# Performance work log

Measured on AMD Instinct MI355X. Metric: run time of the kernel, lower is better.

Reference implementation:

```python
import jax, jax.numpy as jnp
import numpy as np

N, E, G = 50000, 600000, 512
F_IN, H, OUT = 128, 128, 256


def setup_inputs() -> dict:
    key = jax.random.key(0)
    ks = jax.random.split(key, 16)
    x = jax.random.normal(ks[0], (N, F_IN), dtype=jnp.float32)
    edge_index = jax.random.randint(ks[1], (2, E), 0, N, dtype=jnp.int64)
    batch = jnp.sort(jax.random.randint(ks[2], (N,), 0, G, dtype=jnp.int64))
    def lin(k, out_d, in_d):
        s = 1.0 / np.sqrt(in_d)
        return jax.random.uniform(k, (out_d, in_d), jnp.float32, -s, s)
    W1l, W1r = lin(ks[3], H, F_IN), lin(ks[4], H, F_IN)
    b1 = jnp.zeros((H,), jnp.float32)
    W2l, W2r = lin(ks[5], H, H), lin(ks[6], H, H)
    b2 = jnp.zeros((H,), jnp.float32)
    W3l, W3r = lin(ks[7], H, H), lin(ks[8], H, H)
    b3 = jnp.zeros((H,), jnp.float32)
    Wlin = lin(ks[9], OUT, 2 * H)
    blin = jnp.zeros((OUT,), jnp.float32)
    return dict(x=x, edge_index=edge_index, batch=batch,
                W1l=W1l, b1=b1, W1r=W1r, W2l=W2l, b2=b2, W2r=W2r,
                W3l=W3l, b3=b3, W3r=W3r, Wlin=Wlin, blin=blin)


def reference(x, edge_index, batch, W1l, b1, W1r, W2l, b2, W2r, W3l, b3, W3r, Wlin, blin):
    src, dst = edge_index[0], edge_index[1]
    # in-degree of each target node (mean aggregation denominator)
    deg = jax.ops.segment_sum(jnp.ones((E,), x.dtype), dst, num_segments=N)
    deg = jnp.maximum(deg, 1.0)[:, None]

    def sage(h, Wl, bl, Wr):
        # mean-aggregate neighbor features then linear; plus root transform
        agg = jax.ops.segment_sum(h[src], dst, num_segments=N) / deg
        return agg @ Wl.T + bl + h @ Wr.T

    h = jax.nn.relu(sage(x, W1l, b1, W1r))
    h = jax.nn.relu(sage(h, W2l, b2, W2r))
    h = sage(h, W3l, b3, W3r)

    # global max / mean pool per graph
    x_max = jax.ops.segment_max(h, batch, num_segments=G)
    x_max = jnp.where(jnp.isfinite(x_max), x_max, 0.0)
    cnt = jnp.maximum(jax.ops.segment_sum(jnp.ones((N,), h.dtype), batch, num_segments=G), 1.0)
    x_mean = jax.ops.segment_sum(h, batch, num_segments=G) / cnt[:, None]

    pooled = jnp.concatenate([x_max, x_mean], axis=1)  # [G, 2H]
    # dropout is identity in eval mode
    return pooled @ Wlin.T + blin
```

## Files before the change

### kernel.cpp

```cpp
#include <hip/hip_runtime.h>
#include <hip/hip_bf16.h>
#include <hip/hip_fp16.h>


#define FH 128
#define OUTD 256
#define SCHUNK 2048

typedef unsigned int u32;
typedef unsigned short u16;
typedef __attribute__((ext_vector_type(8))) _Float16 f16frag;
typedef __attribute__((ext_vector_type(4))) float f4frag;

typedef __attribute__((address_space(3))) u32 lds_u32;
typedef __attribute__((address_space(1))) const u32 glb_u32;

__device__ inline void async_copy16(const void* g, void* l) {
    __builtin_amdgcn_global_load_lds((glb_u32*)g, (lds_u32*)l, 16, 0, 0);
}

__global__ void prep_all(const float* __restrict__ x, u16* __restrict__ x16, int n4, int PX,
                         const float* __restrict__ W0, const float* __restrict__ W1,
                         const float* __restrict__ W2, const float* __restrict__ W3,
                         const float* __restrict__ W4, const float* __restrict__ W5,
                         uint4* __restrict__ Bf, int PW,
                         const int* __restrict__ dst, int* __restrict__ cnt, int E) {
    int blk = blockIdx.x;
    if (blk < PX) {
        int id = blk * 256 + threadIdx.x;
        if (id >= n4) return;
        float4 v = *(const float4*)(x + (size_t)id * 4);
        __half h0 = __float2half(v.x), h1 = __float2half(v.y);
        __half h2 = __float2half(v.z), h3 = __float2half(v.w);
        ushort4 s;
        s.x = *(u16*)&h0; s.y = *(u16*)&h1; s.z = *(u16*)&h2; s.w = *(u16*)&h3;
        *(ushort4*)(x16 + (size_t)id * 4) = s;
    } else if (blk < PX + PW) {
        int pair = (blk - PX) * 4 + (threadIdx.x >> 6);
        if (pair >= 48) return;
        int ks = pair & 7;
        int arr = pair >> 3;
        int l = threadIdx.x & 63;
        const float* Ws[6] = {W0, W1, W2, W3, W4, W5};
        const float* W = Ws[arr];
        bool use_lo = (ks >= 4);
        int kb = (ks & 3) * 32 + (l >> 4) * 8;
        uint4* out = Bf + (size_t)arr * 4096;
        #pragma unroll
        for (int ot = 0; ot < 8; ++ot) {
            int o = ot * 16 + (l & 15);
            u32 h[8];
            #pragma unroll
            for (int i = 0; i < 8; ++i) {
                float v = W[o * 128 + kb + i];
                __half hi = __float2half(v);
                if (use_lo) {
                    float rem = v - __half2float(hi);
                    __half lo = __float2half(rem);
                    h[i] = *(u16*)&lo;
                } else {
                    h[i] = *(u16*)&hi;
                }
            }
            uint4 u;
            u.x = h[0] | (h[1] << 16);
            u.y = h[2] | (h[3] << 16);
            u.z = h[4] | (h[5] << 16);
            u.w = h[6] | (h[7] << 16);
            out[(ks * 8 + ot) * 64 + l] = u;
        }
    } else {
        int e = (blk - PX - PW) * 256 + threadIdx.x;
        if (e < E) atomicAdd(&cnt[dst[e]], 1);
    }
}

__global__ void scanA_kernel(const int* __restrict__ cnt, int* __restrict__ bsum, int n) {
    __shared__ int ws[4];
    int b = blockIdx.x, t = threadIdx.x;
    int base = b * SCHUNK + t * 8;
    int s = 0;
    #pragma unroll
    for (int k = 0; k < 8; ++k) {
        int i = base + k;
        s += (i < n) ? cnt[i] : 0;
    }
    #pragma unroll
    for (int off = 32; off >= 1; off >>= 1) s += __shfl_xor(s, off, 64);
    int w = t >> 6, lane = t & 63;
    if (lane == 0) ws[w] = s;
    __syncthreads();
    if (t == 0) bsum[b] = ws[0] + ws[1] + ws[2] + ws[3];
}

__global__ void scanC_kernel(const int* __restrict__ cnt, const int* __restrict__ bsum,
                             int NB, int* __restrict__ rp, float* __restrict__ dinv, int n) {
    __shared__ int ws[4];
    __shared__ int base_s;
    int b = blockIdx.x, t = threadIdx.x;
    if (t < 64) {
        int v = (t < NB) ? bsum[t] : 0;
        int pre = (t < b) ? v : 0;
        #pragma unroll
        for (int off = 32; off >= 1; off >>= 1) pre += __shfl_xor(pre, off, 64);
        if (t == 0) base_s = pre;
        if (b == 0) {
            int tot = v;
            #pragma unroll
            for (int off = 32; off >= 1; off >>= 1) tot += __shfl_xor(tot, off, 64);
            if (t == 0) rp[n] = tot;
        }
    }
    __syncthreads();
    int boff = base_s;
    int base = b * SCHUNK + t * 8;
    int v[8];
    int ts = 0;
    #pragma unroll
    for (int k = 0; k < 8; ++k) {
        int i = base + k;
        v[k] = (i < n) ? cnt[i] : 0;
        ts += v[k];
    }
    int w = t >> 6, lane = t & 63;
    int x = ts;
    #pragma unroll
    for (int off = 1; off < 64; off <<= 1) {
        int y = __shfl_up(x, off, 64);
        if (lane >= off) x += y;
    }
    if (lane == 63) ws[w] = x;
    __syncthreads();
    int woff = 0;
    #pragma unroll
    for (int q = 0; q < 4; ++q) woff += (q < w) ? ws[q] : 0;
    int run = boff + woff + (x - ts);
    #pragma unroll
    for (int k = 0; k < 8; ++k) {
        int i = base + k;
        if (i < n) {
            rp[i] = run;
            dinv[i] = 1.0f / (float)max(v[k], 1);
        }
        run += v[k];
    }
}

__global__ void scatter_bounds(const int* __restrict__ src, const int* __restrict__ dst,
                               const int* __restrict__ rp, int* __restrict__ cursor,
                               int* __restrict__ esrc, int E, int SC,
                               const int* __restrict__ batch, int* __restrict__ gstart,
                               int n, int g) {
    int blk = blockIdx.x;
    if (blk < SC) {
        int e = blk * 256 + threadIdx.x;
        if (e < E) {
            int d = dst[e];
            int pos = rp[d] + atomicAdd(&cursor[d], 1);
            esrc[pos] = src[e];
        }
    } else {
        int i = (blk - SC) * 256 + threadIdx.x;
        if (i >= n) return;
        int b = batch[i];
        int pb = (i == 0) ? -1 : batch[i - 1];
        for (int q = pb + 1; q <= b; ++q) gstart[q] = i;
        if (i == n - 1) {
            for (int q = b + 1; q <= g; ++q) gstart[q] = n;
        }
    }
}

__device__ inline void add8(float* a, uint4 u) {
    float2 f0 = __half22float2(*(__half2*)&u.x);
    float2 f1 = __half22float2(*(__half2*)&u.y);
    float2 f2 = __half22float2(*(__half2*)&u.z);
    float2 f3 = __half22float2(*(__half2*)&u.w);
    a[0] += f0.x; a[1] += f0.y; a[2] += f1.x; a[3] += f1.y;
    a[4] += f2.x; a[5] += f2.y; a[6] += f3.x; a[7] += f3.y;
}

__global__ void agg_kernel(const u16* __restrict__ h16,
                           const int* __restrict__ rp, const int* __restrict__ esrc,
                           const float* __restrict__ dinv,
                           u16* __restrict__ agg16, int n_nodes) {
    int node = blockIdx.x * 16 + (threadIdx.x >> 4);
    if (node >= n_nodes) return;
    int lane = threadIdx.x & 15;
    int f = lane * 8;
    int s0 = rp[node], s1 = rp[node + 1];
    float a0[8] = {0, 0, 0, 0, 0, 0, 0, 0};
    float a1[8] = {0, 0, 0, 0, 0, 0, 0, 0};
    float a2[8] = {0, 0, 0, 0, 0, 0, 0, 0};
    float a3[8] = {0, 0, 0, 0, 0, 0, 0, 0};
    int j = s0;
    for (; j + 8 <= s1; j += 8) {
        int i0 = esrc[j],     i1 = esrc[j + 1], i2 = esrc[j + 2], i3 = esrc[j + 3];
        int i4 = esrc[j + 4], i5 = esrc[j + 5], i6 = esrc[j + 6], i7 = esrc[j + 7];
        uint4 u0 = *(const uint4*)(h16 + (size_t)i0 * FH + f);
        uint4 u1 = *(const uint4*)(h16 + (size_t)i1 * FH + f);
        uint4 u2 = *(const uint4*)(h16 + (size_t)i2 * FH + f);
        uint4 u3 = *(const uint4*)(h16 + (size_t)i3 * FH + f);
        uint4 u4 = *(const uint4*)(h16 + (size_t)i4 * FH + f);
        uint4 u5 = *(const uint4*)(h16 + (size_t)i5 * FH + f);
        uint4 u6 = *(const uint4*)(h16 + (size_t)i6 * FH + f);
        uint4 u7 = *(const uint4*)(h16 + (size_t)i7 * FH + f);
        add8(a0, u0); add8(a1, u1); add8(a2, u2); add8(a3, u3);
        add8(a0, u4); add8(a1, u5); add8(a2, u6); add8(a3, u7);
    }
    if (j + 4 <= s1) {
        int i0 = esrc[j], i1 = esrc[j + 1], i2 = esrc[j + 2], i3 = esrc[j + 3];
        uint4 u0 = *(const uint4*)(h16 + (size_t)i0 * FH + f);
        uint4 u1 = *(const uint4*)(h16 + (size_t)i1 * FH + f);
        uint4 u2 = *(const uint4*)(h16 + (size_t)i2 * FH + f);
        uint4 u3 = *(const uint4*)(h16 + (size_t)i3 * FH + f);
        add8(a0, u0); add8(a1, u1); add8(a2, u2); add8(a3, u3);
        j += 4;
    }
    for (; j < s1; ++j) {
        uint4 u0 = *(const uint4*)(h16 + (size_t)esrc[j] * FH + f);
        add8(a0, u0);
    }
    float di = dinv[node];
    u32 oh[8];
    #pragma unroll
    for (int i = 0; i < 8; ++i) {
        __half hv = __float2half((a0[i] + a1[i] + a2[i] + a3[i]) * di);
        oh[i] = *(u16*)&hv;
    }
    uint4 w;
    w.x = oh[0] | (oh[1] << 16);
    w.y = oh[2] | (oh[3] << 16);
    w.z = oh[4] | (oh[5] << 16);
    w.w = oh[6] | (oh[7] << 16);
    *(uint4*)(agg16 + (size_t)node * FH + f) = w;
}

__global__ __launch_bounds__(256, 2)
void mfma_gemm(const u16* __restrict__ A1, const u16* __restrict__ A2,
               const uint4* __restrict__ Bf1, const uint4* __restrict__ Bf2,
               const float* __restrict__ bias, u16* __restrict__ out16,
               int do_relu) {
    __shared__ uint4 Bl[4096];
    int tid = threadIdx.x;
    int l = tid & 63;
    int wv = tid >> 6;
    int bn0 = blockIdx.x * 192 + wv * 48;
    int m = l & 15, q = l >> 4;

    f4frag acc[3][8];
    #pragma unroll
    for (int i = 0; i < 3; ++i)
        #pragma unroll
        for (int o = 0; o < 8; ++o)
            acc[i][o] = (f4frag){0.f, 0.f, 0.f, 0.f};

    #pragma unroll
    for (int p = 0; p < 2; ++p) {
        const u16* P = p ? A2 : A1;
        const uint4* Bf = p ? Bf2 : Bf1;

        f16frag Af[3][4];
        #pragma unroll
        for (int nt = 0; nt < 3; ++nt)
            #pragma unroll
            for (int s = 0; s < 4; ++s)
                Af[nt][s] = *(const f16frag*)(P + (size_t)(bn0 + nt * 16 + m) * FH + s * 32 + q * 8);

        __syncthreads();

        #pragma unroll
        for (int u = 0; u < 16; ++u)
            async_copy16(Bf + (size_t)u * 256 + wv * 64 + l,
                         &Bl[u * 256 + wv * 64]);
        __syncthreads();

        #pragma unroll
        for (int s = 0; s < 4; ++s) {
            {
                f16frag B[8];
                #pragma unroll
                for (int ot = 0; ot < 8; ++ot)
                    B[ot] = *(const f16frag*)&Bl[(size_t)(s * 8 + ot) * 64 + l];
                #pragma unroll
                for (int ot = 0; ot < 8; ++ot)
                    #pragma unroll
                    for (int nt = 0; nt < 3; ++nt)
                        acc[nt][ot] = __builtin_amdgcn_mfma_f32_16x16x32_f16(Af[nt][s], B[ot], acc[nt][ot], 0, 0, 0);
            }
            {
                f16frag B[8];
                #pragma unroll
                for (int ot = 0; ot < 8; ++ot)
                    B[ot] = *(const f16frag*)&Bl[(size_t)((s + 4) * 8 + ot) * 64 + l];
                #pragma unroll
                for (int ot = 0; ot < 8; ++ot)
                    #pragma unroll
                    for (int nt = 0; nt < 3; ++nt)
                        acc[nt][ot] = __builtin_amdgcn_mfma_f32_16x16x32_f16(Af[nt][s], B[ot], acc[nt][ot], 0, 0, 0);
            }
        }
    }

    #pragma unroll
    for (int nt = 0; nt < 3; ++nt)
        #pragma unroll
        for (int r = 0; r < 4; ++r) {
            int node = bn0 + nt * 16 + q * 4 + r;
            #pragma unroll
            for (int ot = 0; ot < 8; ++ot) {
                float v = acc[nt][ot][r] + bias[ot * 16 + m];
                if (do_relu) v = fmaxf(v, 0.f);
                __half hv = __float2half(v);
                out16[(size_t)node * FH + ot * 16 + m] = *(u16*)&hv;
            }
        }
}

__global__ __launch_bounds__(256, 2)
void pool_final(const u16* __restrict__ h16, const int* __restrict__ gstart,
                const float* __restrict__ Wlin, const float* __restrict__ blin,
                float* __restrict__ out) {
    __shared__ float smax[16][FH];
    __shared__ float ssum[16][FH];
    __shared__ float pr[2 * FH];
    int g = blockIdx.x;
    int tid = threadIdx.x;
    int way = tid >> 4;
    int lane = tid & 15;
    int f = lane * 8;
    int s = gstart[g], e = gstart[g + 1];

    float mx[8], sm[8];
    #pragma unroll
    for (int i = 0; i < 8; ++i) { mx[i] = -INFINITY; sm[i] = 0.f; }
    for (int n = s + way; n < e; n += 16) {
        uint4 u = *(const uint4*)(h16 + (size_t)n * FH + f);
        float2 f0 = __half22float2(*(__half2*)&u.x);
        float2 f1 = __half22float2(*(__half2*)&u.y);
        float2 f2 = __half22float2(*(__half2*)&u.z);
        float2 f3 = __half22float2(*(__half2*)&u.w);
        float v[8] = {f0.x, f0.y, f1.x, f1.y, f2.x, f2.y, f3.x, f3.y};
        #pragma unroll
        for (int i = 0; i < 8; ++i) {
            mx[i] = fmaxf(mx[i], v[i]);
            sm[i] += v[i];
        }
    }
    #pragma unroll
    for (int i = 0; i < 8; ++i) {
        smax[way][f + i] = mx[i];
        ssum[way][f + i] = sm[i];
    }
    __syncthreads();
    int c = e - s;
    if (tid < FH) {
        float m2 = -INFINITY, s2 = 0.f;
        #pragma unroll
        for (int w2 = 0; w2 < 16; ++w2) {
            m2 = fmaxf(m2, smax[w2][tid]);
            s2 += ssum[w2][tid];
        }
        pr[tid] = (c > 0) ? m2 : 0.f;
        pr[FH + tid] = s2 / (float)max(c, 1);
    }
    __syncthreads();
    int o = tid;
    const float4* wr = (const float4*)(Wlin + (size_t)o * (2 * FH));
    float acc = 0.f;
    #pragma unroll
    for (int j = 0; j < (2 * FH) / 4; ++j) {
        float4 wv = wr[j];
        acc += wv.x * pr[j * 4 + 0] + wv.y * pr[j * 4 + 1] +
               wv.z * pr[j * 4 + 2] + wv.w * pr[j * 4 + 3];
    }
    out[(size_t)g * OUTD + o] = acc + blin[o];
}

extern "C" void kernel_launch(void* const* d_in, const int* in_sizes, int n_in,
                              void* d_out, int out_size, void* d_ws, size_t ws_size,
                              hipStream_t stream) {
    const float* x     = (const float*)d_in[0];
    const int*   ei    = (const int*)d_in[1];
    const int*   batch = (const int*)d_in[2];
    const float* W1l = (const float*)d_in[3];
    const float* b1  = (const float*)d_in[4];
    const float* W1r = (const float*)d_in[5];
    const float* W2l = (const float*)d_in[6];
    const float* b2  = (const float*)d_in[7];
    const float* W2r = (const float*)d_in[8];
    const float* W3l = (const float*)d_in[9];
    const float* b3  = (const float*)d_in[10];
    const float* W3r = (const float*)d_in[11];
    const float* Wlin = (const float*)d_in[12];
    const float* blin = (const float*)d_in[13];
    float* out = (float*)d_out;

    const int E = in_sizes[1] / 2;
    const int N = in_sizes[2];
    const int G = out_size / OUTD;
    const int* src = ei;
    const int* dst = ei + E;
    const int NB = (N + SCHUNK - 1) / SCHUNK;
    const int GB = (N + 191) / 192;
    const int NP = GB * 192;

    char* w = (char*)d_ws;
    auto alloc = [&](size_t bytes) {
        void* p = (void*)w;
        w += (bytes + 255) & ~(size_t)255;
        return p;
    };
    int*   cnt    = (int*)alloc((size_t)2 * N * sizeof(int));
    int*   cursor = cnt + N;
    int*   rp     = (int*)alloc((size_t)(N + 1) * sizeof(int));
    int*   esrc   = (int*)alloc((size_t)E * sizeof(int));
    int*   gstart = (int*)alloc((size_t)(G + 1) * sizeof(int));
    float* dinv   = (float*)alloc((size_t)N * sizeof(float));
    int*   bsum   = (int*)alloc(64 * sizeof(int));
    u16*   x16    = (u16*)alloc((size_t)NP * FH * sizeof(u16));
    u16*   agg16  = (u16*)alloc((size_t)NP * FH * sizeof(u16));
    u16*   hA16   = (u16*)alloc((size_t)NP * FH * sizeof(u16));
    u16*   hB16   = (u16*)alloc((size_t)NP * FH * sizeof(u16));
    uint4* BF     = (uint4*)alloc((size_t)6 * 4096 * sizeof(uint4));
    (void)ws_size;

    hipMemsetAsync(cnt, 0, (size_t)2 * N * sizeof(int), stream);
    const int n4 = N * 32;
    const int PX = (n4 + 255) / 256;
    const int PW = 12;
    const int PH = (E + 255) / 256;
    prep_all<<<PX + PW + PH, 256, 0, stream>>>(x, x16, n4, PX,
                                               W1l, W1r, W2l, W2r, W3l, W3r, BF, PW,
                                               dst, cnt, E);

    scanA_kernel<<<NB, 256, 0, stream>>>(cnt, bsum, N);
    scanC_kernel<<<NB, 256, 0, stream>>>(cnt, bsum, NB, rp, dinv, N);
    const int SC = (E + 255) / 256;
    const int GBND = (N + 255) / 256;
    scatter_bounds<<<SC + GBND, 256, 0, stream>>>(src, dst, rp, cursor, esrc, E, SC,
                                                  batch, gstart, N, G);

    const int agg_grid = (N + 15) / 16;

    agg_kernel<<<agg_grid, 256, 0, stream>>>(x16, rp, esrc, dinv, agg16, N);
    mfma_gemm<<<GB, 256, 0, stream>>>(agg16, x16, BF + 0 * 4096, BF + 1 * 4096, b1, hA16, 1);
    agg_kernel<<<agg_grid, 256, 0, stream>>>(hA16, rp, esrc, dinv, agg16, N);
    mfma_gemm<<<GB, 256, 0, stream>>>(agg16, hA16, BF + 2 * 4096, BF + 3 * 4096, b2, hB16, 1);
    agg_kernel<<<agg_grid, 256, 0, stream>>>(hB16, rp, esrc, dinv, agg16, N);
    mfma_gemm<<<GB, 256, 0, stream>>>(agg16, hB16, BF + 4 * 4096, BF + 5 * 4096, b3, hA16, 0);

    pool_final<<<G, 256, 0, stream>>>(hA16, gstart, Wlin, blin, out);
}
```

Before: 324.2 us.

## Fuse neighbor aggregation into GEMM kernel via LDS and merge scan kernels

The separate agg_kernel and mfma_gemm launches are merged into one agg_gemm kernel. Each block gathers and mean-aggregates its 192 nodes' neighbor features into swizzled LDS, then runs the MFMA GEMM on that tile. This removes the agg16 global write and read round trip and three launches. The two-pass scan is also collapsed into one kernel, where each block redundantly sums its whole prefix. In exchange, the gather phase now runs at GEMM-sized occupancy with only 261 blocks and 12 serial node passes per wave group, which may hide gather latency less well.

```diff
diff --git a/kernel.cpp b/kernel.cpp
--- a/kernel.cpp
+++ b/kernel.cpp
@@ -75,44 +75,26 @@
     }
 }
 
-__global__ void scanA_kernel(const int* __restrict__ cnt, int* __restrict__ bsum, int n) {
+__global__ void scan_kernel(const int* __restrict__ cnt, int* __restrict__ rp,
+                            float* __restrict__ dinv, int n) {
     __shared__ int ws[4];
     int b = blockIdx.x, t = threadIdx.x;
-    int base = b * SCHUNK + t * 8;
-    int s = 0;
-    #pragma unroll
-    for (int k = 0; k < 8; ++k) {
-        int i = base + k;
-        s += (i < n) ? cnt[i] : 0;
-    }
-    #pragma unroll
-    for (int off = 32; off >= 1; off >>= 1) s += __shfl_xor(s, off, 64);
     int w = t >> 6, lane = t & 63;
-    if (lane == 0) ws[w] = s;
-    __syncthreads();
-    if (t == 0) bsum[b] = ws[0] + ws[1] + ws[2] + ws[3];
-}
-
-__global__ void scanC_kernel(const int* __restrict__ cnt, const int* __restrict__ bsum,
-                             int NB, int* __restrict__ rp, float* __restrict__ dinv, int n) {
-    __shared__ int ws[4];
-    __shared__ int base_s;
-    int b = blockIdx.x, t = threadIdx.x;
-    if (t < 64) {
-        int v = (t < NB) ? bsum[t] : 0;
-        int pre = (t < b) ? v : 0;
-        #pragma unroll
-        for (int off = 32; off >= 1; off >>= 1) pre += __shfl_xor(pre, off, 64);
-        if (t == 0) base_s = pre;
-        if (b == 0) {
-            int tot = v;
-            #pragma unroll
-            for (int off = 32; off >= 1; off >>= 1) tot += __shfl_xor(tot, off, 64);
-            if (t == 0) rp[n] = tot;
-        }
-    }
-    __syncthreads();
-    int boff = base_s;
+
+    int pre = 0;
+    const int4* c4 = (const int4*)cnt;
+    int npre4 = (b * SCHUNK) >> 2;
+    for (int i = t; i < npre4; i += 256) {
+        int4 v = c4[i];
+        pre += v.x + v.y + v.z + v.w;
+    }
+    #pragma unroll
+    for (int off = 32; off >= 1; off >>= 1) pre += __shfl_xor(pre, off, 64);
+    if (lane == 0) ws[w] = pre;
+    __syncthreads();
+    int boff = ws[0] + ws[1] + ws[2] + ws[3];
+    __syncthreads();
+
     int base = b * SCHUNK + t * 8;
     int v[8];
     int ts = 0;
@@ -122,7 +104,6 @@
         v[k] = (i < n) ? cnt[i] : 0;
         ts += v[k];
     }
-    int w = t >> 6, lane = t & 63;
     int x = ts;
     #pragma unroll
     for (int off = 1; off < 64; off <<= 1) {
@@ -144,6 +125,7 @@
         }
         run += v[k];
     }
+    if (b == (int)gridDim.x - 1 && t == 255) rp[n] = run;
 }
 
 __global__ void scatter_bounds(const int* __restrict__ src, const int* __restrict__ dst,
@@ -180,73 +162,91 @@
     a[4] += f2.x; a[5] += f2.y; a[6] += f3.x; a[7] += f3.y;
 }
 
-__global__ void agg_kernel(const u16* __restrict__ h16,
-                           const int* __restrict__ rp, const int* __restrict__ esrc,
-                           const float* __restrict__ dinv,
-                           u16* __restrict__ agg16, int n_nodes) {
-    int node = blockIdx.x * 16 + (threadIdx.x >> 4);
-    if (node >= n_nodes) return;
-    int lane = threadIdx.x & 15;
-    int f = lane * 8;
-    int s0 = rp[node], s1 = rp[node + 1];
-    float a0[8] = {0, 0, 0, 0, 0, 0, 0, 0};
-    float a1[8] = {0, 0, 0, 0, 0, 0, 0, 0};
-    float a2[8] = {0, 0, 0, 0, 0, 0, 0, 0};
-    float a3[8] = {0, 0, 0, 0, 0, 0, 0, 0};
-    int j = s0;
-    for (; j + 8 <= s1; j += 8) {
-        int i0 = esrc[j],     i1 = esrc[j + 1], i2 = esrc[j + 2], i3 = esrc[j + 3];
-        int i4 = esrc[j + 4], i5 = esrc[j + 5], i6 = esrc[j + 6], i7 = esrc[j + 7];
-        uint4 u0 = *(const uint4*)(h16 + (size_t)i0 * FH + f);
-        uint4 u1 = *(const uint4*)(h16 + (size_t)i1 * FH + f);
-        uint4 u2 = *(const uint4*)(h16 + (size_t)i2 * FH + f);
-        uint4 u3 = *(const uint4*)(h16 + (size_t)i3 * FH + f);
-        uint4 u4 = *(const uint4*)(h16 + (size_t)i4 * FH + f);
-        uint4 u5 = *(const uint4*)(h16 + (size_t)i5 * FH + f);
-        uint4 u6 = *(const uint4*)(h16 + (size_t)i6 * FH + f);
-        uint4 u7 = *(const uint4*)(h16 + (size_t)i7 * FH + f);
-        add8(a0, u0); add8(a1, u1); add8(a2, u2); add8(a3, u3);
-        add8(a0, u4); add8(a1, u5); add8(a2, u6); add8(a3, u7);
-    }
-    if (j + 4 <= s1) {
-        int i0 = esrc[j], i1 = esrc[j + 1], i2 = esrc[j + 2], i3 = esrc[j + 3];
-        uint4 u0 = *(const uint4*)(h16 + (size_t)i0 * FH + f);
-        uint4 u1 = *(const uint4*)(h16 + (size_t)i1 * FH + f);
-        uint4 u2 = *(const uint4*)(h16 + (size_t)i2 * FH + f);
-        uint4 u3 = *(const uint4*)(h16 + (size_t)i3 * FH + f);
-        add8(a0, u0); add8(a1, u1); add8(a2, u2); add8(a3, u3);
-        j += 4;
-    }
-    for (; j < s1; ++j) {
-        uint4 u0 = *(const uint4*)(h16 + (size_t)esrc[j] * FH + f);
-        add8(a0, u0);
-    }
-    float di = dinv[node];
-    u32 oh[8];
-    #pragma unroll
-    for (int i = 0; i < 8; ++i) {
-        __half hv = __float2half((a0[i] + a1[i] + a2[i] + a3[i]) * di);
-        oh[i] = *(u16*)&hv;
-    }
-    uint4 w;
-    w.x = oh[0] | (oh[1] << 16);
-    w.y = oh[2] | (oh[3] << 16);
-    w.z = oh[4] | (oh[5] << 16);
-    w.w = oh[6] | (oh[7] << 16);
-    *(uint4*)(agg16 + (size_t)node * FH + f) = w;
-}
-
 __global__ __launch_bounds__(256, 2)
-void mfma_gemm(const u16* __restrict__ A1, const u16* __restrict__ A2,
-               const uint4* __restrict__ Bf1, const uint4* __restrict__ Bf2,
-               const float* __restrict__ bias, u16* __restrict__ out16,
-               int do_relu) {
+void agg_gemm(const u16* __restrict__ H,
+              const int* __restrict__ rp, const int* __restrict__ esrc,
+              const float* __restrict__ dinv,
+              const uint4* __restrict__ Bf1, const uint4* __restrict__ Bf2,
+              const float* __restrict__ bias, u16* __restrict__ out16,
+              int do_relu, int n_nodes) {
     __shared__ uint4 Bl[4096];
+    u16* Al = (u16*)Bl;
     int tid = threadIdx.x;
+    int nbase = blockIdx.x * 192;
+
+    {
+        int way = tid >> 4;
+        int lane16 = tid & 15;
+        int f = lane16 * 8;
+        for (int p = 0; p < 12; ++p) {
+            int nl = p * 16 + way;
+            int node = nbase + nl;
+            int s0 = 0, s1 = 0;
+            float di = 0.f;
+            if (node < n_nodes) { s0 = rp[node]; s1 = rp[node + 1]; di = dinv[node]; }
+            float a0[8] = {0, 0, 0, 0, 0, 0, 0, 0};
+            float a1[8] = {0, 0, 0, 0, 0, 0, 0, 0};
+            float a2[8] = {0, 0, 0, 0, 0, 0, 0, 0};
+            float a3[8] = {0, 0, 0, 0, 0, 0, 0, 0};
+            int j = s0;
+            for (; j + 8 <= s1; j += 8) {
+                int i0 = esrc[j],     i1 = esrc[j + 1], i2 = esrc[j + 2], i3 = esrc[j + 3];
+                int i4 = esrc[j + 4], i5 = esrc[j + 5], i6 = esrc[j + 6], i7 = esrc[j + 7];
+                uint4 u0 = *(const uint4*)(H + (size_t)i0 * FH + f);
+                uint4 u1 = *(const uint4*)(H + (size_t)i1 * FH + f);
+                uint4 u2 = *(const uint4*)(H + (size_t)i2 * FH + f);
+                uint4 u3 = *(const uint4*)(H + (size_t)i3 * FH + f);
+                uint4 u4 = *(const uint4*)(H + (size_t)i4 * FH + f);
+                uint4 u5 = *(const uint4*)(H + (size_t)i5 * FH + f);
+                uint4 u6 = *(const uint4*)(H + (size_t)i6 * FH + f);
+                uint4 u7 = *(const uint4*)(H + (size_t)i7 * FH + f);
+                add8(a0, u0); add8(a1, u1); add8(a2, u2); add8(a3, u3);
+                add8(a0, u4); add8(a1, u5); add8(a2, u6); add8(a3, u7);
+            }
+            if (j + 4 <= s1) {
+                int i0 = esrc[j], i1 = esrc[j + 1], i2 = esrc[j + 2], i3 = esrc[j + 3];
+                uint4 u0 = *(const uint4*)(H + (size_t)i0 * FH + f);
+                uint4 u1 = *(const uint4*)(H + (size_t)i1 * FH + f);
+                uint4 u2 = *(const uint4*)(H + (size_t)i2 * FH + f);
+                uint4 u3 = *(const uint4*)(H + (size_t)i3 * FH + f);
+                add8(a0, u0); add8(a1, u1); add8(a2, u2); add8(a3, u3);
+                j += 4;
+            }
+            for (; j < s1; ++j) {
+                uint4 u0 = *(const uint4*)(H + (size_t)esrc[j] * FH + f);
+                add8(a0, u0);
+            }
+            u32 oh[8];
+            #pragma unroll
+            for (int i = 0; i < 8; ++i) {
+                __half hv = __float2half((a0[i] + a1[i] + a2[i] + a3[i]) * di);
+                oh[i] = *(u16*)&hv;
+            }
+            uint4 wv4;
+            wv4.x = oh[0] | (oh[1] << 16);
+            wv4.y = oh[2] | (oh[3] << 16);
+            wv4.z = oh[4] | (oh[5] << 16);
+            wv4.w = oh[6] | (oh[7] << 16);
+            int byte = (nl * 256 + lane16 * 16) ^ ((nl & 7) << 4);
+            *(uint4*)((char*)Al + byte) = wv4;
+        }
+    }
+    __syncthreads();
+
     int l = tid & 63;
     int wv = tid >> 6;
-    int bn0 = blockIdx.x * 192 + wv * 48;
+    int bn0 = nbase + wv * 48;
     int m = l & 15, q = l >> 4;
+
+    f16frag Af[3][4];
+    #pragma unroll
+    for (int nt = 0; nt < 3; ++nt)
+        #pragma unroll
+        for (int s = 0; s < 4; ++s) {
+            int nl = wv * 48 + nt * 16 + m;
+            int byte = (nl * 256 + s * 64 + q * 16) ^ ((nl & 7) << 4);
+            Af[nt][s] = *(const f16frag*)((const char*)Al + byte);
+        }
 
     f4frag acc[3][8];
     #pragma unroll
@@ -255,50 +255,78 @@
         for (int o = 0; o < 8; ++o)
             acc[i][o] = (f4frag){0.f, 0.f, 0.f, 0.f};
 
-    #pragma unroll
-    for (int p = 0; p < 2; ++p) {
-        const u16* P = p ? A2 : A1;
-        const uint4* Bf = p ? Bf2 : Bf1;
-
-        f16frag Af[3][4];
-        #pragma unroll
-        for (int nt = 0; nt < 3; ++nt)
-            #pragma unroll
-            for (int s = 0; s < 4; ++s)
-                Af[nt][s] = *(const f16frag*)(P + (size_t)(bn0 + nt * 16 + m) * FH + s * 32 + q * 8);
-
-        __syncthreads();
-
-        #pragma unroll
-        for (int u = 0; u < 16; ++u)
-            async_copy16(Bf + (size_t)u * 256 + wv * 64 + l,
-                         &Bl[u * 256 + wv * 64]);
-        __syncthreads();
-
-        #pragma unroll
-        for (int s = 0; s < 4; ++s) {
-            {
-                f16frag B[8];
+    __syncthreads();
+
+    #pragma unroll
+    for (int u = 0; u < 16; ++u)
+        async_copy16(Bf1 + (size_t)u * 256 + wv * 64 + l,
+                     &Bl[u * 256 + wv * 64]);
+    __syncthreads();
+
+    #pragma unroll
+    for (int s = 0; s < 4; ++s) {
+        {
+            f16frag B[8];
+            #pragma unroll
+            for (int ot = 0; ot < 8; ++ot)
+                B[ot] = *(const f16frag*)&Bl[(size_t)(s * 8 + ot) * 64 + l];
+            #pragma unroll
+            for (int ot = 0; ot < 8; ++ot)
                 #pragma unroll
-                for (int ot = 0; ot < 8; ++ot)
-                    B[ot] = *(const f16frag*)&Bl[(size_t)(s * 8 + ot) * 64 + l];
+                for (int nt = 0; nt < 3; ++nt)
+                    acc[nt][ot] = __builtin_amdgcn_mfma_f32_16x16x32_f16(Af[nt][s], B[ot], acc[nt][ot], 0, 0, 0);
+        }
+        {
+            f16frag B[8];
+            #pragma unroll
+            for (int ot = 0; ot < 8; ++ot)
+                B[ot] = *(const f16frag*)&Bl[(size_t)((s + 4) * 8 + ot) * 64 + l];
+            #pragma unroll
+            for (int ot = 0; ot < 8; ++ot)
                 #pragma unroll
-                for (int ot = 0; ot < 8; ++ot)
-                    #pragma unroll
-                    for (int nt = 0; nt < 3; ++nt)
-                        acc[nt][ot] = __builtin_amdgcn_mfma_f32_16x16x32_f16(Af[nt][s], B[ot], acc[nt][ot], 0, 0, 0);
-            }
-            {
-                f16frag B[8];
+                for (int nt = 0; nt < 3; ++nt)
+                    acc[nt][ot] = __builtin_amdgcn_mfma_f32_16x16x32_f16(Af[nt][s], B[ot], acc[nt][ot], 0, 0, 0);
+        }
+    }
+
+    f16frag Ag[3][4];
+    #pragma unroll
+    for (int nt = 0; nt < 3; ++nt)
+        #pragma unroll
+        for (int s = 0; s < 4; ++s)
+            Ag[nt][s] = *(const f16frag*)(H + (size_t)(bn0 + nt * 16 + m) * FH + s * 32 + q * 8);
+
+    __syncthreads();
+
+    #pragma unroll
+    for (int u = 0; u < 16; ++u)
+        async_copy16(Bf2 + (size_t)u * 256 + wv * 64 + l,
+                     &Bl[u * 256 + wv * 64]);
+    __syncthreads();
+
+    #pragma unroll
+    for (int s = 0; s < 4; ++s) {
+        {
+            f16frag B[8];
+            #pragma unroll
+            for (int ot = 0; ot < 8; ++ot)
+                B[ot] = *(const f16frag*)&Bl[(size_t)(s * 8 + ot) * 64 + l];
+            #pragma unroll
+            for (int ot = 0; ot < 8; ++ot)
                 #pragma unroll
-                for (int ot = 0; ot < 8; ++ot)
-                    B[ot] = *(const f16frag*)&Bl[(size_t)((s + 4) * 8 + ot) * 64 + l];
+                for (int nt = 0; nt < 3; ++nt)
+                    acc[nt][ot] = __builtin_amdgcn_mfma_f32_16x16x32_f16(Ag[nt][s], B[ot], acc[nt][ot], 0, 0, 0);
+        }
+        {
+            f16frag B[8];
+            #pragma unroll
+            for (int ot = 0; ot < 8; ++ot)
+                B[ot] = *(const f16frag*)&Bl[(size_t)((s + 4) * 8 + ot) * 64 + l];
+            #pragma unroll
+            for (int ot = 0; ot < 8; ++ot)
                 #pragma unroll
-                for (int ot = 0; ot < 8; ++ot)
-                    #pragma unroll
-                    for (int nt = 0; nt < 3; ++nt)
-                        acc[nt][ot] = __builtin_amdgcn_mfma_f32_16x16x32_f16(Af[nt][s], B[ot], acc[nt][ot], 0, 0, 0);
-            }
+                for (int nt = 0; nt < 3; ++nt)
+                    acc[nt][ot] = __builtin_amdgcn_mfma_f32_16x16x32_f16(Ag[nt][s], B[ot], acc[nt][ot], 0, 0, 0);
         }
     }
 
@@ -417,9 +445,7 @@
     int*   esrc   = (int*)alloc((size_t)E * sizeof(int));
     int*   gstart = (int*)alloc((size_t)(G + 1) * sizeof(int));
     float* dinv   = (float*)alloc((size_t)N * sizeof(float));
-    int*   bsum   = (int*)alloc(64 * sizeof(int));
     u16*   x16    = (u16*)alloc((size_t)NP * FH * sizeof(u16));
-    u16*   agg16  = (u16*)alloc((size_t)NP * FH * sizeof(u16));
     u16*   hA16   = (u16*)alloc((size_t)NP * FH * sizeof(u16));
     u16*   hB16   = (u16*)alloc((size_t)NP * FH * sizeof(u16));
     uint4* BF     = (uint4*)alloc((size_t)6 * 4096 * sizeof(uint4));
@@ -434,21 +460,15 @@
                                                W1l, W1r, W2l, W2r, W3l, W3r, BF, PW,
                                                dst, cnt, E);
 
-    scanA_kernel<<<NB, 256, 0, stream>>>(cnt, bsum, N);
-    scanC_kernel<<<NB, 256, 0, stream>>>(cnt, bsum, NB, rp, dinv, N);
+    scan_kernel<<<NB, 256, 0, stream>>>(cnt, rp, dinv, N);
     const int SC = (E + 255) / 256;
     const int GBND = (N + 255) / 256;
     scatter_bounds<<<SC + GBND, 256, 0, stream>>>(src, dst, rp, cursor, esrc, E, SC,
                                                   batch, gstart, N, G);
 
-    const int agg_grid = (N + 15) / 16;
-
-    agg_kernel<<<agg_grid, 256, 0, stream>>>(x16, rp, esrc, dinv, agg16, N);
-    mfma_gemm<<<GB, 256, 0, stream>>>(agg16, x16, BF + 0 * 4096, BF + 1 * 4096, b1, hA16, 1);
-    agg_kernel<<<agg_grid, 256, 0, stream>>>(hA16, rp, esrc, dinv, agg16, N);
-    mfma_gemm<<<GB, 256, 0, stream>>>(agg16, hA16, BF + 2 * 4096, BF + 3 * 4096, b2, hB16, 1);
-    agg_kernel<<<agg_grid, 256, 0, stream>>>(hB16, rp, esrc, dinv, agg16, N);
-    mfma_gemm<<<GB, 256, 0, stream>>>(agg16, hB16, BF + 4 * 4096, BF + 5 * 4096, b3, hA16, 0);
+    agg_gemm<<<GB, 256, 0, stream>>>(x16,  rp, esrc, dinv, BF + 0 * 4096, BF + 1 * 4096, b1, hA16, 1, N);
+    agg_gemm<<<GB, 256, 0, stream>>>(hA16, rp, esrc, dinv, BF + 2 * 4096, BF + 3 * 4096, b2, hB16, 1, N);
+    agg_gemm<<<GB, 256, 0, stream>>>(hB16, rp, esrc, dinv, BF + 4 * 4096, BF + 5 * 4096, b3, hA16, 0, N);
 
     pool_final<<<G, 256, 0, stream>>>(hA16, gstart, Wlin, blin, out);
 }
```

Measured after the change: 395.0 us. +21.8%, slower.

## Merge two-pass scan into one kernel and read GEMM weights from global directly

Applied to the files above, without the earlier changes.

The two scan kernels become one: each block sums all preceding counts itself (redundant prefix reads over at most ~50K ints) instead of going through a separate block-sum pass, which saves one launch. The GEMM drops the LDS staging of the weight fragments, so the async copy and both barriers are gone, and B fragments are loaded straight from global memory, relying on L1/L2 since every block reads the same 64KB of weights. The risk is higher global load latency inside the MFMA loop, set against lower LDS use and possibly higher occupancy.

```diff
diff --git a/kernel.cpp b/kernel.cpp
--- a/kernel.cpp
+++ b/kernel.cpp
@@ -11,13 +11,6 @@
 typedef unsigned short u16;
 typedef __attribute__((ext_vector_type(8))) _Float16 f16frag;
 typedef __attribute__((ext_vector_type(4))) float f4frag;
-
-typedef __attribute__((address_space(3))) u32 lds_u32;
-typedef __attribute__((address_space(1))) const u32 glb_u32;
-
-__device__ inline void async_copy16(const void* g, void* l) {
-    __builtin_amdgcn_global_load_lds((glb_u32*)g, (lds_u32*)l, 16, 0, 0);
-}
 
 __global__ void prep_all(const float* __restrict__ x, u16* __restrict__ x16, int n4, int PX,
                          const float* __restrict__ W0, const float* __restrict__ W1,
@@ -75,44 +68,26 @@
     }
 }
 
-__global__ void scanA_kernel(const int* __restrict__ cnt, int* __restrict__ bsum, int n) {
+__global__ void scan_kernel(const int* __restrict__ cnt, int* __restrict__ rp,
+                            float* __restrict__ dinv, int n) {
     __shared__ int ws[4];
     int b = blockIdx.x, t = threadIdx.x;
-    int base = b * SCHUNK + t * 8;
-    int s = 0;
-    #pragma unroll
-    for (int k = 0; k < 8; ++k) {
-        int i = base + k;
-        s += (i < n) ? cnt[i] : 0;
-    }
-    #pragma unroll
-    for (int off = 32; off >= 1; off >>= 1) s += __shfl_xor(s, off, 64);
     int w = t >> 6, lane = t & 63;
-    if (lane == 0) ws[w] = s;
+
+    int pre = 0;
+    const int4* c4 = (const int4*)cnt;
+    int npre4 = (b * SCHUNK) >> 2;
+    for (int i = t; i < npre4; i += 256) {
+        int4 v = c4[i];
+        pre += v.x + v.y + v.z + v.w;
+    }
+    #pragma unroll
+    for (int off = 32; off >= 1; off >>= 1) pre += __shfl_xor(pre, off, 64);
+    if (lane == 0) ws[w] = pre;
     __syncthreads();
-    if (t == 0) bsum[b] = ws[0] + ws[1] + ws[2] + ws[3];
-}
-
-__global__ void scanC_kernel(const int* __restrict__ cnt, const int* __restrict__ bsum,
-                             int NB, int* __restrict__ rp, float* __restrict__ dinv, int n) {
-    __shared__ int ws[4];
-    __shared__ int base_s;
-    int b = blockIdx.x, t = threadIdx.x;
-    if (t < 64) {
-        int v = (t < NB) ? bsum[t] : 0;
-        int pre = (t < b) ? v : 0;
-        #pragma unroll
-        for (int off = 32; off >= 1; off >>= 1) pre += __shfl_xor(pre, off, 64);
-        if (t == 0) base_s = pre;
-        if (b == 0) {
-            int tot = v;
-            #pragma unroll
-            for (int off = 32; off >= 1; off >>= 1) tot += __shfl_xor(tot, off, 64);
-            if (t == 0) rp[n] = tot;
-        }
-    }
+    int boff = ws[0] + ws[1] + ws[2] + ws[3];
     __syncthreads();
-    int boff = base_s;
+
     int base = b * SCHUNK + t * 8;
     int v[8];
     int ts = 0;
@@ -122,7 +97,6 @@
         v[k] = (i < n) ? cnt[i] : 0;
         ts += v[k];
     }
-    int w = t >> 6, lane = t & 63;
     int x = ts;
     #pragma unroll
     for (int off = 1; off < 64; off <<= 1) {
@@ -144,6 +118,7 @@
         }
         run += v[k];
     }
+    if (b == (int)gridDim.x - 1 && t == 255) rp[n] = run;
 }
 
 __global__ void scatter_bounds(const int* __restrict__ src, const int* __restrict__ dst,
@@ -241,7 +216,6 @@
                const uint4* __restrict__ Bf1, const uint4* __restrict__ Bf2,
                const float* __restrict__ bias, u16* __restrict__ out16,
                int do_relu) {
-    __shared__ uint4 Bl[4096];
     int tid = threadIdx.x;
     int l = tid & 63;
     int wv = tid >> 6;
@@ -267,32 +241,14 @@
             for (int s = 0; s < 4; ++s)
                 Af[nt][s] = *(const f16frag*)(P + (size_t)(bn0 + nt * 16 + m) * FH + s * 32 + q * 8);
 
-        __syncthreads();
-
-        #pragma unroll
-        for (int u = 0; u < 16; ++u)
-            async_copy16(Bf + (size_t)u * 256 + wv * 64 + l,
-                         &Bl[u * 256 + wv * 64]);
-        __syncthreads();
-
         #pragma unroll
         for (int s = 0; s < 4; ++s) {
-            {
+            #pragma unroll
+            for (int ph = 0; ph < 2; ++ph) {
                 f16frag B[8];
                 #pragma unroll
                 for (int ot = 0; ot < 8; ++ot)
-                    B[ot] = *(const f16frag*)&Bl[(size_t)(s * 8 + ot) * 64 + l];
-                #pragma unroll
-                for (int ot = 0; ot < 8; ++ot)
-                    #pragma unroll
-                    for (int nt = 0; nt < 3; ++nt)
-                        acc[nt][ot] = __builtin_amdgcn_mfma_f32_16x16x32_f16(Af[nt][s], B[ot], acc[nt][ot], 0, 0, 0);
-            }
-            {
-                f16frag B[8];
-                #pragma unroll
-                for (int ot = 0; ot < 8; ++ot)
-                    B[ot] = *(const f16frag*)&Bl[(size_t)((s + 4) * 8 + ot) * 64 + l];
+                    B[ot] = *(const f16frag*)&Bf[(size_t)((s + ph * 4) * 8 + ot) * 64 + l];
                 #pragma unroll
                 for (int ot = 0; ot < 8; ++ot)
                     #pragma unroll
@@ -417,7 +373,6 @@
     int*   esrc   = (int*)alloc((size_t)E * sizeof(int));
     int*   gstart = (int*)alloc((size_t)(G + 1) * sizeof(int));
     float* dinv   = (float*)alloc((size_t)N * sizeof(float));
-    int*   bsum   = (int*)alloc(64 * sizeof(int));
     u16*   x16    = (u16*)alloc((size_t)NP * FH * sizeof(u16));
     u16*   agg16  = (u16*)alloc((size_t)NP * FH * sizeof(u16));
     u16*   hA16   = (u16*)alloc((size_t)NP * FH * sizeof(u16));
@@ -434,8 +389,7 @@
                                                W1l, W1r, W2l, W2r, W3l, W3r, BF, PW,
                                                dst, cnt, E);
 
-    scanA_kernel<<<NB, 256, 0, stream>>>(cnt, bsum, N);
-    scanC_kernel<<<NB, 256, 0, stream>>>(cnt, bsum, NB, rp, dinv, N);
+    scan_kernel<<<NB, 256, 0, stream>>>(cnt, rp, dinv, N);
     const int SC = (E + 255) / 256;
     const int GBND = (N + 255) / 256;
     scatter_bounds<<<SC + GBND, 256, 0, stream>>>(src, dst, rp, cursor, esrc, E, SC,
```

After: 378.3 us. 16.7% more time.
